# Optimization experiments

Hardware: AMD Instinct MI355X
Metric: run time of the kernel (lower is better)

## Reference

```python
import jax, jax.numpy as jnp
import numpy as np

N_HEAD = 16
HEAD_DIM = 64
N_EMBD = N_HEAD * HEAD_DIM
KS, STRIDE = 4, 4
LN_EPS = 1e-5


def _layernorm(x, g, b):
    mu = jnp.mean(x, axis=-1, keepdims=True)
    var = jnp.var(x, axis=-1, keepdims=True)
    return (x - mu) * jax.lax.rsqrt(var + LN_EPS) * g + b


def _depthwise_conv(x_bcl, w):
    # x_bcl: [N, head_dim, L], w: [head_dim, 1, KS] (torch Conv1d groups=head_dim layout)
    return jax.lax.conv_general_dilated(
        x_bcl, w, window_strides=(STRIDE,), padding='VALID',
        dimension_numbers=('NCH', 'OIH', 'NCH'), feature_group_count=HEAD_DIM)


def setup_inputs() -> dict:
    key = jax.random.key(0)
    ks = jax.random.split(key, 12)
    B, T, L = 8, 64, 4096
    s = 0.02
    return {
        'x': jax.random.normal(ks[0], (B, T, N_EMBD), jnp.float32),
        'cached_k': jax.random.normal(ks[1], (B, N_HEAD, L, HEAD_DIM), jnp.float32),
        'cached_v': jax.random.normal(ks[2], (B, N_HEAD, L, HEAD_DIM), jnp.float32),
        'w_attn': jax.random.normal(ks[3], (N_EMBD, 3 * N_EMBD), jnp.float32) * s,
        'b_attn': jnp.zeros((3 * N_EMBD,), jnp.float32),
        'w_proj': jax.random.normal(ks[4], (N_EMBD, N_EMBD), jnp.float32) * s,
        'b_proj': jnp.zeros((N_EMBD,), jnp.float32),
        'k_conv': jax.random.normal(ks[5], (HEAD_DIM, 1, KS), jnp.float32) * 0.5,
        'v_conv': jax.random.normal(ks[6], (HEAD_DIM, 1, KS), jnp.float32) * 0.5,
        'ln_k_g': jnp.ones((HEAD_DIM,), jnp.float32),
        'ln_k_b': jnp.zeros((HEAD_DIM,), jnp.float32),
        'ln_v_g': jnp.ones((HEAD_DIM,), jnp.float32),
        'ln_v_b': jnp.zeros((HEAD_DIM,), jnp.float32),
    }


def reference(x, cached_k, cached_v, w_attn, b_attn, w_proj, b_proj,
              k_conv, v_conv, ln_k_g, ln_k_b, ln_v_g, ln_v_b):
    B, T, C = x.shape
    H, hd = N_HEAD, HEAD_DIM
    qkv = x @ w_attn + b_attn                      # [B,T,3C]
    q, k, v = jnp.split(qkv, 3, axis=-1)
    q = q.reshape(B, T, H, hd).transpose(0, 2, 1, 3)  # [B,H,T,hd]
    k = k.reshape(B, T, H, hd).transpose(0, 2, 1, 3)
    v = v.reshape(B, T, H, hd).transpose(0, 2, 1, 3)

    # compress cached K/V: depthwise conv over cache length, then LayerNorm
    L = cached_k.shape[2]
    pk = cached_k.transpose(0, 1, 3, 2).reshape(B * H, hd, L)
    pv = cached_v.transpose(0, 1, 3, 2).reshape(B * H, hd, L)
    ck = _depthwise_conv(pk, k_conv).reshape(B, H, hd, -1).transpose(0, 1, 3, 2)  # [B,H,Lc,hd]
    cv = _depthwise_conv(pv, v_conv).reshape(B, H, hd, -1).transpose(0, 1, 3, 2)
    ck = jax.lax.stop_gradient(_layernorm(ck, ln_k_g, ln_k_b))
    cv = jax.lax.stop_gradient(_layernorm(cv, ln_v_g, ln_v_b))

    k_full = jnp.concatenate([ck, k], axis=2)      # [B,H,Tk,hd]
    v_full = jnp.concatenate([cv, v], axis=2)
    Tk = k_full.shape[2]

    # faithful to original: rectangular tril(T, Tk) -> query i sees keys j<=i
    mask = jnp.tril(jnp.ones((T, Tk), dtype=bool))
    att = jnp.einsum('bhqd,bhkd->bhqk', q, k_full) * (1.0 / np.sqrt(hd))
    att = jnp.where(mask[None, None], att, -jnp.inf)
    att = jax.nn.softmax(att, axis=-1)
    y = jnp.einsum('bhqk,bhkd->bhqd', att, v_full)
    y = y.transpose(0, 2, 1, 3).reshape(B, T, C)
    return y @ w_proj + b_proj
```

## Files before the change

### kernel.cpp

```cpp
#include <hip/hip_runtime.h>
#include <math.h>

#define NH 16
#define LCACHE 4096

typedef __attribute__((ext_vector_type(8))) short short8;
typedef __attribute__((ext_vector_type(8))) unsigned short ushort8;
typedef __attribute__((ext_vector_type(4))) float f32x4;

__device__ __forceinline__ unsigned short f2bf(float f) {
    unsigned int u = __float_as_uint(f);
    u = (u + 0x7fffu + ((u >> 16) & 1u)) >> 16;
    return (unsigned short)u;
}

__global__ __launch_bounds__(256)
void prep_kernel(const float* __restrict__ cached_k, const float* __restrict__ cached_v,
                 const float* __restrict__ kcw, const float* __restrict__ vcw,
                 const float* __restrict__ lkg, const float* __restrict__ lkb,
                 const float* __restrict__ lvg, const float* __restrict__ lvb,
                 const float* __restrict__ x, const float* __restrict__ w_attn,
                 const float* __restrict__ w_proj,
                 ushort* __restrict__ ckf, ushort* __restrict__ cvtf,
                 ushort* __restrict__ xp, ushort* __restrict__ wq,
                 ushort* __restrict__ wp)
{
    __shared__ float Wt[64][65];
    const int bid = blockIdx.x, tid = threadIdx.x;
    const int w = tid >> 6, l = tid & 63;

    const int bh = bid >> 2, sub = bid & 3;
    const int T = sub >> 1, half = sub & 1;
    const float* S = (T ? cached_v : cached_k) + (size_t)bh * (LCACHE * 64);
    float tap[8][4];
#pragma unroll
    for (int rq = 0; rq < 8; ++rq) {
        int key = half * 32 + w * 8 + rq;
        const float* p = S + (size_t)key * 256 + l;
        tap[rq][0] = p[0]; tap[rq][1] = p[64]; tap[rq][2] = p[128]; tap[rq][3] = p[192];
    }

    const int isP = (bid >= 256);
    const int g2  = bid & 255;
    const int ntw = g2 >> 4, ktw = g2 & 15;
    const float* W = isP ? w_proj : w_attn;
    const int ldw  = isP ? 1024 : 3072;
    ushort* D      = isP ? wp : wq;
    float wreg[16];
#pragma unroll
    for (int rep = 0; rep < 16; ++rep) {
        int lin = rep * 256 + tid;
        int kr = lin >> 6, nn = lin & 63;
        wreg[rep] = W[(size_t)(ktw * 64 + kr) * ldw + ntw * 64 + nn];
    }

    {
        const float* cwp = T ? vcw : kcw;
        float4 w4v = *(const float4*)(cwp + l * 4);
        float g = (T ? lvg : lkg)[l], bb = (T ? lvb : lkb)[l];
        ushort* dstf = (T ? cvtf : ckf) + (size_t)bh * 4096;
#pragma unroll
        for (int it = 0; it < 2; ++it) {
            float av[4];
#pragma unroll
            for (int q = 0; q < 4; ++q) {
                int rq = it * 4 + q;
                float acc = tap[rq][0] * w4v.x;
                acc = fmaf(tap[rq][1], w4v.y, acc);
                acc = fmaf(tap[rq][2], w4v.z, acc);
                acc = fmaf(tap[rq][3], w4v.w, acc);
                av[q] = acc;
            }
            float s1[4], s2[4];
#pragma unroll
            for (int q = 0; q < 4; ++q) { s1[q] = av[q]; s2[q] = av[q] * av[q]; }
#pragma unroll
            for (int o = 32; o; o >>= 1) {
#pragma unroll
                for (int q = 0; q < 4; ++q) {
                    s1[q] += __shfl_xor(s1[q], o);
                    s2[q] += __shfl_xor(s2[q], o);
                }
            }
#pragma unroll
            for (int q = 0; q < 4; ++q) {
                int key = half * 32 + w * 8 + it * 4 + q;
                float mu  = s1[q] * 0.015625f;
                float var = s2[q] * 0.015625f - mu * mu;
                float outv = (av[q] - mu) * rsqrtf(var + 1e-5f) * g + bb;
                const int d = l;
                int off;
                if (T)
                    off = ((d >> 4) * 2 + (key >> 5)) * 512
                        + ((key >> 3) & 3) * 128 + (d & 15) * 8 + (key & 7);
                else
                    off = ((key >> 4) * 2 + (d >> 5)) * 512
                        + ((d >> 3) & 3) * 128 + (key & 15) * 8 + (d & 7);
                dstf[off] = f2bf(outv);
            }
        }
    }

    {
#pragma unroll
        for (int rep = 0; rep < 16; ++rep) {
            int lin = rep * 256 + tid;
            Wt[lin >> 6][lin & 63] = wreg[rep];
        }
        __syncthreads();
        int r = l & 15, kg8 = l >> 4;
#pragma unroll
        for (int e = 0; e < 2; ++e) {
            int bi = w + e * 4;
            int kb = bi >> 2, nb = bi & 3;
            ushort8 o;
#pragma unroll
            for (int j = 0; j < 8; ++j)
                o[j] = f2bf(Wt[kb * 32 + kg8 * 8 + j][nb * 16 + r]);
            size_t f_lin = (size_t)(ntw * 16 + ktw) * 8 + bi;
            *(ushort8*)(D + f_lin * 512 + l * 8) = o;
        }
    }

    if (bid < 64) {
        int r = l & 15, kg8 = l >> 4;
#pragma unroll
        for (int i = 0; i < 4; ++i) {
            int f = bid * 16 + w * 4 + i;
            int mt = f >> 6, kt = (f >> 2) & 15, fi = f & 3;
            int kb = fi >> 1, mb = fi & 1;
            int m  = mt * 32 + mb * 16 + r;
            int k0 = kt * 64 + kb * 32 + kg8 * 8;
            const float* s = x + (size_t)m * 1024 + k0;
            ushort8 o;
#pragma unroll
            for (int j = 0; j < 8; ++j) o[j] = f2bf(s[j]);
            *(ushort8*)(xp + (size_t)f * 512 + l * 8) = o;
        }
    }
}

__global__ __launch_bounds__(512, 2)
void attn_kernel(const ushort* __restrict__ ckf, const ushort* __restrict__ cvtf,
                 const float* __restrict__ b_attn,
                 const ushort* __restrict__ xp, const ushort* __restrict__ wq,
                 ushort* __restrict__ yp)
{
    __shared__ __align__(16) float qs[32][68];
    __shared__ __align__(16) ushort P_lds[32 * 64];

    const int bid = blockIdx.x;
    const int h    = ((bid & 7) << 1) | ((bid >> 3) & 1);
    const int rem  = bid >> 4;
    const int b    = rem >> 1;
    const int half = rem & 1;
    const int mtA  = b * 2 + half;

    const int tid = threadIdx.x;
    const int w = tid >> 6, l = tid & 63;
    const int kg = w >> 2, w4 = w & 3;
    const int c = l & 15, rg = l >> 4;
    const int g = w & 1, dup = w >> 1;

    const ushort* ckb = ckf + (size_t)(b * NH + h) * 4096;
    const ushort* cvb = cvtf + (size_t)(b * NH + h) * 4096;
    short8 akf[4][2];
#pragma unroll
    for (int mf = 0; mf < 4; ++mf)
#pragma unroll
        for (int kf = 0; kf < 2; ++kf)
            akf[mf][kf] = *(const short8*)(ckb + (mf * 2 + kf) * 512 + l * 8);
    short8 avf[2];
#pragma unroll
    for (int kf = 0; kf < 2; ++kf)
        avf[kf] = *(const short8*)(cvb + (dup * 2 + kf) * 512 + l * 8);

    const ushort* ab = xp + (size_t)mtA * 32768;
    const ushort* bb = wq + (size_t)h * 65536;
    f32x4 acc0 = {0.f,0.f,0.f,0.f}, acc1 = {0.f,0.f,0.f,0.f};
#pragma unroll
    for (int s = 0; s < 8; ++s) {
        const int kt = kg * 8 + s;
        const ushort* A = ab + kt * 2048;
        const ushort* B = bb + kt * 4096;
        short8 a00 = *(const short8*)(A + l * 8);
        short8 a01 = *(const short8*)(A + 512 + l * 8);
        short8 a10 = *(const short8*)(A + 1024 + l * 8);
        short8 a11 = *(const short8*)(A + 1536 + l * 8);
        short8 b0  = *(const short8*)(B + (size_t)w4 * 512 + l * 8);
        short8 b1  = *(const short8*)(B + (size_t)(4 + w4) * 512 + l * 8);
        acc0 = __builtin_amdgcn_mfma_f32_16x16x32_bf16(a00, b0, acc0, 0, 0, 0);
        acc1 = __builtin_amdgcn_mfma_f32_16x16x32_bf16(a01, b0, acc1, 0, 0, 0);
        acc0 = __builtin_amdgcn_mfma_f32_16x16x32_bf16(a10, b1, acc0, 0, 0, 0);
        acc1 = __builtin_amdgcn_mfma_f32_16x16x32_bf16(a11, b1, acc1, 0, 0, 0);
    }

    {
        const int n = w4 * 16 + c;
        if (kg == 0) {
#pragma unroll
            for (int mb = 0; mb < 2; ++mb) {
                f32x4 acc = mb ? acc1 : acc0;
#pragma unroll
                for (int rr = 0; rr < 4; ++rr)
                    qs[mb * 16 + rg * 4 + rr][n] = acc[rr];
            }
        }
        __syncthreads();
        if (kg == 1) {
            float bv = b_attn[h * 64 + n];
#pragma unroll
            for (int mb = 0; mb < 2; ++mb) {
                f32x4 acc = mb ? acc1 : acc0;
#pragma unroll
                for (int rr = 0; rr < 4; ++rr) {
                    int m = mb * 16 + rg * 4 + rr;
                    qs[m][n] = (qs[m][n] + acc[rr] + bv) * 0.125f;
                }
            }
        }
        __syncthreads();
    }

    short8 qb[2];
#pragma unroll
    for (int kf = 0; kf < 2; ++kf) {
        int row = 16 * g + c;
        int d0  = 32 * kf + 8 * rg;
        float4 v0 = *(const float4*)&qs[row][d0];
        float4 v1 = *(const float4*)&qs[row][d0 + 4];
        ushort8 t;
        t[0] = f2bf(v0.x); t[1] = f2bf(v0.y); t[2] = f2bf(v0.z); t[3] = f2bf(v0.w);
        t[4] = f2bf(v1.x); t[5] = f2bf(v1.y); t[6] = f2bf(v1.z); t[7] = f2bf(v1.w);
        qb[kf] = (short8)t;
    }

    f32x4 sacc[4];
#pragma unroll
    for (int mf = 0; mf < 4; ++mf) { sacc[mf][0]=0.f; sacc[mf][1]=0.f; sacc[mf][2]=0.f; sacc[mf][3]=0.f; }
#pragma unroll
    for (int mf = 0; mf < 4; ++mf) {
        sacc[mf] = __builtin_amdgcn_mfma_f32_16x16x32_bf16(akf[mf][0], qb[0], sacc[mf], 0, 0, 0);
        sacc[mf] = __builtin_amdgcn_mfma_f32_16x16x32_bf16(akf[mf][1], qb[1], sacc[mf], 0, 0, 0);
    }

    const int gq = half * 32 + 16 * g + c;
    float pv[4][4];
    float mx = -3.0e38f;
#pragma unroll
    for (int mf = 0; mf < 4; ++mf)
#pragma unroll
        for (int rr = 0; rr < 4; ++rr) {
            int kidx = 16 * mf + 4 * rg + rr;
            float sc = (kidx <= gq) ? sacc[mf][rr] : -3.0e38f;
            pv[mf][rr] = sc;
            mx = fmaxf(mx, sc);
        }
    mx = fmaxf(mx, __shfl_xor(mx, 16));
    mx = fmaxf(mx, __shfl_xor(mx, 32));
    float sum = 0.f;
#pragma unroll
    for (int mf = 0; mf < 4; ++mf)
#pragma unroll
        for (int rr = 0; rr < 4; ++rr) {
            int kidx = 16 * mf + 4 * rg + rr;
            float e = (kidx <= gq) ? __expf(pv[mf][rr] - mx) : 0.f;
            pv[mf][rr] = e;
            sum += e;
        }
    sum += __shfl_xor(sum, 16);
    sum += __shfl_xor(sum, 32);
    float inv = 1.0f / sum;

    if (dup == 0) {
        int q = 16 * g + c;
        int swz = (q & 7) << 3;
#pragma unroll
        for (int mf = 0; mf < 4; ++mf)
#pragma unroll
            for (int rr = 0; rr < 4; ++rr) {
                int kidx = 16 * mf + 4 * rg + rr;
                P_lds[q * 64 + (kidx ^ swz)] = f2bf(pv[mf][rr] * inv);
            }
    }
    __syncthreads();

    short8 pb[2];
#pragma unroll
    for (int kf = 0; kf < 2; ++kf) {
        int q = 16 * g + c;
        int key0 = 32 * kf + 8 * rg;
        pb[kf] = *(const short8*)&P_lds[q * 64 + (key0 ^ ((q & 7) << 3))];
    }
    f32x4 oacc = {0.f, 0.f, 0.f, 0.f};
    oacc = __builtin_amdgcn_mfma_f32_16x16x32_bf16(avf[0], pb[0], oacc, 0, 0, 0);
    oacc = __builtin_amdgcn_mfma_f32_16x16x32_bf16(avf[1], pb[1], oacc, 0, 0, 0);

#pragma unroll
    for (int rr = 0; rr < 4; ++rr) {
        int d  = 16 * dup + 4 * rg + rr;
        int kb = d >> 5, ke = d & 31;
        int l2 = ((ke >> 3) << 4) | c;
        int j2 = ke & 7;
        size_t off = (size_t)mtA * 32768 + (size_t)h * 2048
                   + (size_t)(kb * 2 + g) * 512 + (size_t)l2 * 8 + j2;
        yp[off] = f2bf(oacc[rr]);
    }
}

__global__ __launch_bounds__(512, 2)
void gemm2_kernel(const ushort* __restrict__ Ap, const ushort* __restrict__ Bp,
                  const float* __restrict__ bias, float* __restrict__ C)
{
    __shared__ float red[32][68];

    const int bid = blockIdx.x;
    const int nt = ((bid & 7) << 1) | ((bid >> 3) & 1);
    const int mt = bid >> 4;
    const int tid = threadIdx.x;
    const int w = tid >> 6, l = tid & 63;
    const int kg = w >> 2, w4 = w & 3;
    const int c = l & 15, rg = l >> 4;

    const ushort* ab = Ap + (size_t)mt * 32768;
    const ushort* bb = Bp + (size_t)nt * 65536;
    f32x4 acc0 = {0.f,0.f,0.f,0.f}, acc1 = {0.f,0.f,0.f,0.f};
#pragma unroll
    for (int s = 0; s < 8; ++s) {
        const int kt = kg * 8 + s;
        const ushort* A = ab + kt * 2048;
        const ushort* B = bb + kt * 4096;
        short8 a00 = *(const short8*)(A + l * 8);
        short8 a01 = *(const short8*)(A + 512 + l * 8);
        short8 a10 = *(const short8*)(A + 1024 + l * 8);
        short8 a11 = *(const short8*)(A + 1536 + l * 8);
        short8 b0  = *(const short8*)(B + (size_t)w4 * 512 + l * 8);
        short8 b1  = *(const short8*)(B + (size_t)(4 + w4) * 512 + l * 8);
        acc0 = __builtin_amdgcn_mfma_f32_16x16x32_bf16(a00, b0, acc0, 0, 0, 0);
        acc1 = __builtin_amdgcn_mfma_f32_16x16x32_bf16(a01, b0, acc1, 0, 0, 0);
        acc0 = __builtin_amdgcn_mfma_f32_16x16x32_bf16(a10, b1, acc0, 0, 0, 0);
        acc1 = __builtin_amdgcn_mfma_f32_16x16x32_bf16(a11, b1, acc1, 0, 0, 0);
    }

    const int nl = w4 * 16 + c;
    if (kg == 0) {
#pragma unroll
        for (int mb = 0; mb < 2; ++mb) {
            f32x4 acc = mb ? acc1 : acc0;
#pragma unroll
            for (int rr = 0; rr < 4; ++rr)
                red[mb * 16 + rg * 4 + rr][nl] = acc[rr];
        }
    }
    __syncthreads();
    if (kg == 1) {
        float bv = bias[nt * 64 + nl];
#pragma unroll
        for (int mb = 0; mb < 2; ++mb) {
            f32x4 acc = mb ? acc1 : acc0;
#pragma unroll
            for (int rr = 0; rr < 4; ++rr) {
                int m = mb * 16 + rg * 4 + rr;
                C[(size_t)(mt * 32 + m) * 1024 + nt * 64 + nl] =
                    red[m][nl] + acc[rr] + bv;
            }
        }
    }
}

extern "C" void kernel_launch(void* const* d_in, const int* in_sizes, int n_in,
                              void* d_out, int out_size, void* d_ws, size_t ws_size,
                              hipStream_t stream)
{
    const float* x        = (const float*)d_in[0];
    const float* cached_k = (const float*)d_in[1];
    const float* cached_v = (const float*)d_in[2];
    const float* w_attn   = (const float*)d_in[3];
    const float* b_attn   = (const float*)d_in[4];
    const float* w_proj   = (const float*)d_in[5];
    const float* b_proj   = (const float*)d_in[6];
    const float* k_conv   = (const float*)d_in[7];
    const float* v_conv   = (const float*)d_in[8];
    const float* ln_k_g   = (const float*)d_in[9];
    const float* ln_k_b   = (const float*)d_in[10];
    const float* ln_v_g   = (const float*)d_in[11];
    const float* ln_v_b   = (const float*)d_in[12];

    ushort* xp   = (ushort*)d_ws;
    ushort* wq   = xp + 524288;
    ushort* wp   = wq + 1048576;
    ushort* yp   = wp + 1048576;
    ushort* ckf  = yp + 524288;
    ushort* cvtf = ckf + 524288;
    float* out   = (float*)d_out;

    prep_kernel<<<512, 256, 0, stream>>>(cached_k, cached_v, k_conv, v_conv,
                                         ln_k_g, ln_k_b, ln_v_g, ln_v_b,
                                         x, w_attn, w_proj, ckf, cvtf, xp, wq, wp);
    attn_kernel<<<256, 512, 0, stream>>>(ckf, cvtf, b_attn, xp, wq, yp);
    gemm2_kernel<<<256, 512, 0, stream>>>(yp, wp, b_proj, out);
}
```

Baseline: 26.88 us.

## Fuse cache conv+LayerNorm into attention kernel, overlapped with Q projection

Moves the depthwise conv and LayerNorm of the cached K/V into the attention kernel. Half the warps compute the compressed keys directly into LDS while the other half compute the Q projection GEMM over the full K dimension, so the split-K reduction through shared memory goes away. Each block computes only the rows it needs (32 or 64 keys depending on half), which removes the global round-trip of the packed ckf/cvtf buffers. The prep kernel becomes a pure weight and activation packing kernel with separate blocks for x. In exchange it adds 16 KB of LDS per block and gives each GEMM warp twice the serial K loop.

```diff
diff --git a/kernel.cpp b/kernel.cpp
--- a/kernel.cpp
+++ b/kernel.cpp
@@ -15,13 +15,8 @@
 }
 
 __global__ __launch_bounds__(256)
-void prep_kernel(const float* __restrict__ cached_k, const float* __restrict__ cached_v,
-                 const float* __restrict__ kcw, const float* __restrict__ vcw,
-                 const float* __restrict__ lkg, const float* __restrict__ lkb,
-                 const float* __restrict__ lvg, const float* __restrict__ lvb,
-                 const float* __restrict__ x, const float* __restrict__ w_attn,
+void pack_kernel(const float* __restrict__ x, const float* __restrict__ w_attn,
                  const float* __restrict__ w_proj,
-                 ushort* __restrict__ ckf, ushort* __restrict__ cvtf,
                  ushort* __restrict__ xp, ushort* __restrict__ wq,
                  ushort* __restrict__ wp)
 {
@@ -29,83 +24,18 @@
     const int bid = blockIdx.x, tid = threadIdx.x;
     const int w = tid >> 6, l = tid & 63;
 
-    const int bh = bid >> 2, sub = bid & 3;
-    const int T = sub >> 1, half = sub & 1;
-    const float* S = (T ? cached_v : cached_k) + (size_t)bh * (LCACHE * 64);
-    float tap[8][4];
-#pragma unroll
-    for (int rq = 0; rq < 8; ++rq) {
-        int key = half * 32 + w * 8 + rq;
-        const float* p = S + (size_t)key * 256 + l;
-        tap[rq][0] = p[0]; tap[rq][1] = p[64]; tap[rq][2] = p[128]; tap[rq][3] = p[192];
-    }
-
-    const int isP = (bid >= 256);
-    const int g2  = bid & 255;
-    const int ntw = g2 >> 4, ktw = g2 & 15;
-    const float* W = isP ? w_proj : w_attn;
-    const int ldw  = isP ? 1024 : 3072;
-    ushort* D      = isP ? wp : wq;
-    float wreg[16];
-#pragma unroll
-    for (int rep = 0; rep < 16; ++rep) {
-        int lin = rep * 256 + tid;
-        int kr = lin >> 6, nn = lin & 63;
-        wreg[rep] = W[(size_t)(ktw * 64 + kr) * ldw + ntw * 64 + nn];
-    }
-
-    {
-        const float* cwp = T ? vcw : kcw;
-        float4 w4v = *(const float4*)(cwp + l * 4);
-        float g = (T ? lvg : lkg)[l], bb = (T ? lvb : lkb)[l];
-        ushort* dstf = (T ? cvtf : ckf) + (size_t)bh * 4096;
-#pragma unroll
-        for (int it = 0; it < 2; ++it) {
-            float av[4];
-#pragma unroll
-            for (int q = 0; q < 4; ++q) {
-                int rq = it * 4 + q;
-                float acc = tap[rq][0] * w4v.x;
-                acc = fmaf(tap[rq][1], w4v.y, acc);
-                acc = fmaf(tap[rq][2], w4v.z, acc);
-                acc = fmaf(tap[rq][3], w4v.w, acc);
-                av[q] = acc;
-            }
-            float s1[4], s2[4];
-#pragma unroll
-            for (int q = 0; q < 4; ++q) { s1[q] = av[q]; s2[q] = av[q] * av[q]; }
-#pragma unroll
-            for (int o = 32; o; o >>= 1) {
-#pragma unroll
-                for (int q = 0; q < 4; ++q) {
-                    s1[q] += __shfl_xor(s1[q], o);
-                    s2[q] += __shfl_xor(s2[q], o);
-                }
-            }
-#pragma unroll
-            for (int q = 0; q < 4; ++q) {
-                int key = half * 32 + w * 8 + it * 4 + q;
-                float mu  = s1[q] * 0.015625f;
-                float var = s2[q] * 0.015625f - mu * mu;
-                float outv = (av[q] - mu) * rsqrtf(var + 1e-5f) * g + bb;
-                const int d = l;
-                int off;
-                if (T)
-                    off = ((d >> 4) * 2 + (key >> 5)) * 512
-                        + ((key >> 3) & 3) * 128 + (d & 15) * 8 + (key & 7);
-                else
-                    off = ((key >> 4) * 2 + (d >> 5)) * 512
-                        + ((d >> 3) & 3) * 128 + (key & 15) * 8 + (d & 7);
-                dstf[off] = f2bf(outv);
-            }
-        }
-    }
-
-    {
+    if (bid < 512) {
+        const int isP = (bid >= 256);
+        const int g2  = bid & 255;
+        const int ntw = g2 >> 4, ktw = g2 & 15;
+        const float* W = isP ? w_proj : w_attn;
+        const int ldw  = isP ? 1024 : 3072;
+        ushort* D      = isP ? wp : wq;
 #pragma unroll
         for (int rep = 0; rep < 16; ++rep) {
             int lin = rep * 256 + tid;
-            Wt[lin >> 6][lin & 63] = wreg[rep];
+            int kr = lin >> 6, nn = lin & 63;
+            Wt[kr][nn] = W[(size_t)(ktw * 64 + kr) * ldw + ntw * 64 + nn];
         }
         __syncthreads();
         int r = l & 15, kg8 = l >> 4;
@@ -120,13 +50,15 @@
             size_t f_lin = (size_t)(ntw * 16 + ktw) * 8 + bi;
             *(ushort8*)(D + f_lin * 512 + l * 8) = o;
         }
-    }
-
-    if (bid < 64) {
+        return;
+    }
+
+    {
+        int bid2 = bid - 512;
         int r = l & 15, kg8 = l >> 4;
 #pragma unroll
         for (int i = 0; i < 4; ++i) {
-            int f = bid * 16 + w * 4 + i;
+            int f = bid2 * 16 + w * 4 + i;
             int mt = f >> 6, kt = (f >> 2) & 15, fi = f & 3;
             int kb = fi >> 1, mb = fi & 1;
             int m  = mt * 32 + mb * 16 + r;
@@ -141,13 +73,18 @@
 }
 
 __global__ __launch_bounds__(512, 2)
-void attn_kernel(const ushort* __restrict__ ckf, const ushort* __restrict__ cvtf,
+void attn_kernel(const float* __restrict__ cached_k, const float* __restrict__ cached_v,
+                 const float* __restrict__ kcw, const float* __restrict__ vcw,
+                 const float* __restrict__ lkg, const float* __restrict__ lkb,
+                 const float* __restrict__ lvg, const float* __restrict__ lvb,
                  const float* __restrict__ b_attn,
                  const ushort* __restrict__ xp, const ushort* __restrict__ wq,
                  ushort* __restrict__ yp)
 {
     __shared__ __align__(16) float qs[32][68];
-    __shared__ __align__(16) ushort P_lds[32 * 64];
+    __shared__ __align__(16) ushort P_lds[2048];
+    __shared__ __align__(16) ushort ckf_s[4096];
+    __shared__ __align__(16) ushort cvf_s[4096];
 
     const int bid = blockIdx.x;
     const int h    = ((bid & 7) << 1) | ((bid >> 3) & 1);
@@ -158,69 +95,115 @@
 
     const int tid = threadIdx.x;
     const int w = tid >> 6, l = tid & 63;
-    const int kg = w >> 2, w4 = w & 3;
     const int c = l & 15, rg = l >> 4;
     const int g = w & 1, dup = w >> 1;
 
-    const ushort* ckb = ckf + (size_t)(b * NH + h) * 4096;
-    const ushort* cvb = cvtf + (size_t)(b * NH + h) * 4096;
+    {
+        ushort8 z = {0,0,0,0,0,0,0,0};
+        ((ushort8*)ckf_s)[tid] = z;
+        ((ushort8*)cvf_s)[tid] = z;
+    }
+    __syncthreads();
+
+    if (w >= 4) {
+        const int cw = w - 4;
+        const int NR = half ? 64 : 32;
+        const float* Kb = cached_k + (size_t)(b * NH + h) * (LCACHE * 64);
+        const float* Vb = cached_v + (size_t)(b * NH + h) * (LCACHE * 64);
+        float4 wk = *(const float4*)(kcw + l * 4);
+        float4 wv = *(const float4*)(vcw + l * 4);
+        float gk = lkg[l], bk = lkb[l], gv = lvg[l], bv = lvb[l];
+
+        const int iters = (2 * NR) / 4;
+        for (int it = 0; it < iters; it += 4) {
+            float tap[4][4]; int isKv[4], lcv[4];
+#pragma unroll
+            for (int q = 0; q < 4; ++q) {
+                int t = cw + (it + q) * 4;
+                isKv[q] = (t < NR);
+                int lc = isKv[q] ? t : t - NR;
+                lcv[q] = lc;
+                const float* p = (isKv[q] ? Kb : Vb) + (size_t)lc * 256 + l;
+                tap[q][0] = p[0]; tap[q][1] = p[64]; tap[q][2] = p[128]; tap[q][3] = p[192];
+            }
+            float av[4], s1[4], s2[4];
+#pragma unroll
+            for (int q = 0; q < 4; ++q) {
+                float4 cwv = isKv[q] ? wk : wv;
+                float a = tap[q][0] * cwv.x;
+                a = fmaf(tap[q][1], cwv.y, a);
+                a = fmaf(tap[q][2], cwv.z, a);
+                a = fmaf(tap[q][3], cwv.w, a);
+                av[q] = a; s1[q] = a; s2[q] = a * a;
+            }
+#pragma unroll
+            for (int o = 32; o; o >>= 1) {
+#pragma unroll
+                for (int q = 0; q < 4; ++q) {
+                    s1[q] += __shfl_xor(s1[q], o);
+                    s2[q] += __shfl_xor(s2[q], o);
+                }
+            }
+#pragma unroll
+            for (int q = 0; q < 4; ++q) {
+                float mu  = s1[q] * 0.015625f;
+                float var = s2[q] * 0.015625f - mu * mu;
+                float gg = isKv[q] ? gk : gv, bb2 = isKv[q] ? bk : bv;
+                float outv = (av[q] - mu) * rsqrtf(var + 1e-5f) * gg + bb2;
+                unsigned short bf = f2bf(outv);
+                int key = lcv[q], d = l;
+                if (isKv[q]) {
+                    int off = ((key >> 4) * 2 + (d >> 5)) * 512
+                            + ((d >> 3) & 3) * 128 + (key & 15) * 8 + (d & 7);
+                    ckf_s[off] = bf;
+                } else {
+                    int off = ((d >> 4) * 2 + (key >> 5)) * 512
+                            + ((key >> 3) & 3) * 128 + (d & 15) * 8 + (key & 7);
+                    cvf_s[off] = bf;
+                }
+            }
+        }
+    } else {
+        const ushort* ab = xp + (size_t)mtA * 32768;
+        const ushort* bb = wq + (size_t)h * 65536;
+        f32x4 acc0 = {0.f,0.f,0.f,0.f}, acc1 = {0.f,0.f,0.f,0.f};
+#pragma unroll
+        for (int kt = 0; kt < 16; ++kt) {
+            const ushort* A = ab + kt * 2048;
+            const ushort* B = bb + kt * 4096;
+            short8 a00 = *(const short8*)(A + l * 8);
+            short8 a01 = *(const short8*)(A + 512 + l * 8);
+            short8 a10 = *(const short8*)(A + 1024 + l * 8);
+            short8 a11 = *(const short8*)(A + 1536 + l * 8);
+            short8 b0  = *(const short8*)(B + (size_t)w * 512 + l * 8);
+            short8 b1  = *(const short8*)(B + (size_t)(4 + w) * 512 + l * 8);
+            acc0 = __builtin_amdgcn_mfma_f32_16x16x32_bf16(a00, b0, acc0, 0, 0, 0);
+            acc1 = __builtin_amdgcn_mfma_f32_16x16x32_bf16(a01, b0, acc1, 0, 0, 0);
+            acc0 = __builtin_amdgcn_mfma_f32_16x16x32_bf16(a10, b1, acc0, 0, 0, 0);
+            acc1 = __builtin_amdgcn_mfma_f32_16x16x32_bf16(a11, b1, acc1, 0, 0, 0);
+        }
+        const int n = w * 16 + c;
+        float bv2 = b_attn[h * 64 + n];
+#pragma unroll
+        for (int mb = 0; mb < 2; ++mb) {
+            f32x4 acc = mb ? acc1 : acc0;
+#pragma unroll
+            for (int rr = 0; rr < 4; ++rr)
+                qs[mb * 16 + rg * 4 + rr][n] = (acc[rr] + bv2) * 0.125f;
+        }
+    }
+    __syncthreads();
+
     short8 akf[4][2];
 #pragma unroll
     for (int mf = 0; mf < 4; ++mf)
 #pragma unroll
         for (int kf = 0; kf < 2; ++kf)
-            akf[mf][kf] = *(const short8*)(ckb + (mf * 2 + kf) * 512 + l * 8);
+            akf[mf][kf] = *(const short8*)&ckf_s[(mf * 2 + kf) * 512 + l * 8];
     short8 avf[2];
 #pragma unroll
     for (int kf = 0; kf < 2; ++kf)
-        avf[kf] = *(const short8*)(cvb + (dup * 2 + kf) * 512 + l * 8);
-
-    const ushort* ab = xp + (size_t)mtA * 32768;
-    const ushort* bb = wq + (size_t)h * 65536;
-    f32x4 acc0 = {0.f,0.f,0.f,0.f}, acc1 = {0.f,0.f,0.f,0.f};
-#pragma unroll
-    for (int s = 0; s < 8; ++s) {
-        const int kt = kg * 8 + s;
-        const ushort* A = ab + kt * 2048;
-        const ushort* B = bb + kt * 4096;
-        short8 a00 = *(const short8*)(A + l * 8);
-        short8 a01 = *(const short8*)(A + 512 + l * 8);
-        short8 a10 = *(const short8*)(A + 1024 + l * 8);
-        short8 a11 = *(const short8*)(A + 1536 + l * 8);
-        short8 b0  = *(const short8*)(B + (size_t)w4 * 512 + l * 8);
-        short8 b1  = *(const short8*)(B + (size_t)(4 + w4) * 512 + l * 8);
-        acc0 = __builtin_amdgcn_mfma_f32_16x16x32_bf16(a00, b0, acc0, 0, 0, 0);
-        acc1 = __builtin_amdgcn_mfma_f32_16x16x32_bf16(a01, b0, acc1, 0, 0, 0);
-        acc0 = __builtin_amdgcn_mfma_f32_16x16x32_bf16(a10, b1, acc0, 0, 0, 0);
-        acc1 = __builtin_amdgcn_mfma_f32_16x16x32_bf16(a11, b1, acc1, 0, 0, 0);
-    }
-
-    {
-        const int n = w4 * 16 + c;
-        if (kg == 0) {
-#pragma unroll
-            for (int mb = 0; mb < 2; ++mb) {
-                f32x4 acc = mb ? acc1 : acc0;
-#pragma unroll
-                for (int rr = 0; rr < 4; ++rr)
-                    qs[mb * 16 + rg * 4 + rr][n] = acc[rr];
-            }
-        }
-        __syncthreads();
-        if (kg == 1) {
-            float bv = b_attn[h * 64 + n];
-#pragma unroll
-            for (int mb = 0; mb < 2; ++mb) {
-                f32x4 acc = mb ? acc1 : acc0;
-#pragma unroll
-                for (int rr = 0; rr < 4; ++rr) {
-                    int m = mb * 16 + rg * 4 + rr;
-                    qs[m][n] = (qs[m][n] + acc[rr] + bv) * 0.125f;
-                }
-            }
-        }
-        __syncthreads();
-    }
+        avf[kf] = *(const short8*)&cvf_s[(dup * 2 + kf) * 512 + l * 8];
 
     short8 qb[2];
 #pragma unroll
@@ -386,17 +369,15 @@
     const float* ln_v_g   = (const float*)d_in[11];
     const float* ln_v_b   = (const float*)d_in[12];
 
-    ushort* xp   = (ushort*)d_ws;
-    ushort* wq   = xp + 524288;
-    ushort* wp   = wq + 1048576;
-    ushort* yp   = wp + 1048576;
-    ushort* ckf  = yp + 524288;
-    ushort* cvtf = ckf + 524288;
-    float* out   = (float*)d_out;
-
-    prep_kernel<<<512, 256, 0, stream>>>(cached_k, cached_v, k_conv, v_conv,
+    ushort* xp = (ushort*)d_ws;
+    ushort* wq = xp + 524288;
+    ushort* wp = wq + 1048576;
+    ushort* yp = wp + 1048576;
+    float* out = (float*)d_out;
+
+    pack_kernel<<<576, 256, 0, stream>>>(x, w_attn, w_proj, xp, wq, wp);
+    attn_kernel<<<256, 512, 0, stream>>>(cached_k, cached_v, k_conv, v_conv,
                                          ln_k_g, ln_k_b, ln_v_g, ln_v_b,
-                                         x, w_attn, w_proj, ckf, cvtf, xp, wq, wp);
-    attn_kernel<<<256, 512, 0, stream>>>(ckf, cvtf, b_attn, xp, wq, yp);
+                                         b_attn, xp, wq, yp);
     gemm2_kernel<<<256, 512, 0, stream>>>(yp, wp, b_proj, out);
 }
```

Measured after the change: 30.09 us. 1.12x slower.

## Split prep and output-projection work across twice as many blocks

Applied to the files above, without the earlier changes.

The prep kernel now launches 1024 blocks, each handling a quarter of the keys, half of a weight tile, and one x fragment per block, so the x conversion is spread across blocks instead of piled onto the first 64. The output-projection GEMM launches 512 blocks with 32-column tiles and a four-way K split, reduced through shared memory. The bf16 conversion switches to the HIP intrinsic. The goal is more parallelism and better latency hiding on a small problem, at the cost of more blocks and a wider reduction.

```diff
diff --git a/kernel.cpp b/kernel.cpp
--- a/kernel.cpp
+++ b/kernel.cpp
@@ -1,4 +1,5 @@
 #include <hip/hip_runtime.h>
+#include <hip/hip_bf16.h>
 #include <math.h>
 
 #define NH 16
@@ -9,12 +10,13 @@
 typedef __attribute__((ext_vector_type(4))) float f32x4;
 
 __device__ __forceinline__ unsigned short f2bf(float f) {
-    unsigned int u = __float_as_uint(f);
-    u = (u + 0x7fffu + ((u >> 16) & 1u)) >> 16;
-    return (unsigned short)u;
+    __hip_bfloat16 b = __float2bfloat16(f);
+    unsigned short u;
+    __builtin_memcpy(&u, &b, 2);
+    return u;
 }
 
-__global__ __launch_bounds__(256)
+__global__ __launch_bounds__(256, 4)
 void prep_kernel(const float* __restrict__ cached_k, const float* __restrict__ cached_v,
                  const float* __restrict__ kcw, const float* __restrict__ vcw,
                  const float* __restrict__ lkg, const float* __restrict__ lkb,
@@ -25,33 +27,47 @@
                  ushort* __restrict__ xp, ushort* __restrict__ wq,
                  ushort* __restrict__ wp)
 {
-    __shared__ float Wt[64][65];
+    __shared__ float Wt[32][65];
     const int bid = blockIdx.x, tid = threadIdx.x;
     const int w = tid >> 6, l = tid & 63;
 
-    const int bh = bid >> 2, sub = bid & 3;
-    const int T = sub >> 1, half = sub & 1;
+    const int bh = bid >> 3, sub = bid & 7;
+    const int T = sub >> 2, quarter = sub & 3;
     const float* S = (T ? cached_v : cached_k) + (size_t)bh * (LCACHE * 64);
-    float tap[8][4];
-#pragma unroll
-    for (int rq = 0; rq < 8; ++rq) {
-        int key = half * 32 + w * 8 + rq;
+    float tap[4][4];
+#pragma unroll
+    for (int q = 0; q < 4; ++q) {
+        int key = quarter * 16 + w * 4 + q;
         const float* p = S + (size_t)key * 256 + l;
-        tap[rq][0] = p[0]; tap[rq][1] = p[64]; tap[rq][2] = p[128]; tap[rq][3] = p[192];
-    }
-
-    const int isP = (bid >= 256);
-    const int g2  = bid & 255;
-    const int ntw = g2 >> 4, ktw = g2 & 15;
+        tap[q][0] = p[0]; tap[q][1] = p[64]; tap[q][2] = p[128]; tap[q][3] = p[192];
+    }
+
+    const int isP = bid >> 9;
+    const int rem = bid & 511;
+    const int ntw = rem >> 5, ktw = (rem >> 1) & 15, kbh = rem & 1;
     const float* W = isP ? w_proj : w_attn;
     const int ldw  = isP ? 1024 : 3072;
     ushort* D      = isP ? wp : wq;
-    float wreg[16];
-#pragma unroll
-    for (int rep = 0; rep < 16; ++rep) {
+    float wreg[8];
+#pragma unroll
+    for (int rep = 0; rep < 8; ++rep) {
         int lin = rep * 256 + tid;
         int kr = lin >> 6, nn = lin & 63;
-        wreg[rep] = W[(size_t)(ktw * 64 + kr) * ldw + ntw * 64 + nn];
+        wreg[rep] = W[(size_t)(ktw * 64 + kbh * 32 + kr) * ldw + ntw * 64 + nn];
+    }
+
+    const int doX = (w == (bid & 3));
+    float xr[8];
+    if (doX) {
+        int f = bid;
+        int mt = f >> 6, kt = (f >> 2) & 15, fi = f & 3;
+        int kb = fi >> 1, mb = fi & 1;
+        int r = l & 15, kg8 = l >> 4;
+        int m  = mt * 32 + mb * 16 + r;
+        int k0 = kt * 64 + kb * 32 + kg8 * 8;
+        const float* s = x + (size_t)m * 1024 + k0;
+#pragma unroll
+        for (int j = 0; j < 8; ++j) xr[j] = s[j];
     }
 
     {
@@ -59,84 +75,63 @@
         float4 w4v = *(const float4*)(cwp + l * 4);
         float g = (T ? lvg : lkg)[l], bb = (T ? lvb : lkb)[l];
         ushort* dstf = (T ? cvtf : ckf) + (size_t)bh * 4096;
-#pragma unroll
-        for (int it = 0; it < 2; ++it) {
-            float av[4];
+        float av[4], s1[4], s2[4];
+#pragma unroll
+        for (int q = 0; q < 4; ++q) {
+            float a = tap[q][0] * w4v.x;
+            a = fmaf(tap[q][1], w4v.y, a);
+            a = fmaf(tap[q][2], w4v.z, a);
+            a = fmaf(tap[q][3], w4v.w, a);
+            av[q] = a; s1[q] = a; s2[q] = a * a;
+        }
+#pragma unroll
+        for (int o = 32; o; o >>= 1) {
 #pragma unroll
             for (int q = 0; q < 4; ++q) {
-                int rq = it * 4 + q;
-                float acc = tap[rq][0] * w4v.x;
-                acc = fmaf(tap[rq][1], w4v.y, acc);
-                acc = fmaf(tap[rq][2], w4v.z, acc);
-                acc = fmaf(tap[rq][3], w4v.w, acc);
-                av[q] = acc;
+                s1[q] += __shfl_xor(s1[q], o);
+                s2[q] += __shfl_xor(s2[q], o);
             }
-            float s1[4], s2[4];
-#pragma unroll
-            for (int q = 0; q < 4; ++q) { s1[q] = av[q]; s2[q] = av[q] * av[q]; }
-#pragma unroll
-            for (int o = 32; o; o >>= 1) {
-#pragma unroll
-                for (int q = 0; q < 4; ++q) {
-                    s1[q] += __shfl_xor(s1[q], o);
-                    s2[q] += __shfl_xor(s2[q], o);
-                }
-            }
-#pragma unroll
-            for (int q = 0; q < 4; ++q) {
-                int key = half * 32 + w * 8 + it * 4 + q;
-                float mu  = s1[q] * 0.015625f;
-                float var = s2[q] * 0.015625f - mu * mu;
-                float outv = (av[q] - mu) * rsqrtf(var + 1e-5f) * g + bb;
-                const int d = l;
-                int off;
-                if (T)
-                    off = ((d >> 4) * 2 + (key >> 5)) * 512
-                        + ((key >> 3) & 3) * 128 + (d & 15) * 8 + (key & 7);
-                else
-                    off = ((key >> 4) * 2 + (d >> 5)) * 512
-                        + ((d >> 3) & 3) * 128 + (key & 15) * 8 + (d & 7);
-                dstf[off] = f2bf(outv);
-            }
+        }
+#pragma unroll
+        for (int q = 0; q < 4; ++q) {
+            int key = quarter * 16 + w * 4 + q;
+            float mu  = s1[q] * 0.015625f;
+            float var = s2[q] * 0.015625f - mu * mu;
+            float outv = (av[q] - mu) * rsqrtf(var + 1e-5f) * g + bb;
+            unsigned short bf = f2bf(outv);
+            const int d = l;
+            int off;
+            if (T)
+                off = ((d >> 4) * 2 + (key >> 5)) * 512
+                    + ((key >> 3) & 3) * 128 + (d & 15) * 8 + (key & 7);
+            else
+                off = ((key >> 4) * 2 + (d >> 5)) * 512
+                    + ((d >> 3) & 3) * 128 + (key & 15) * 8 + (d & 7);
+            dstf[off] = bf;
         }
     }
 
     {
 #pragma unroll
-        for (int rep = 0; rep < 16; ++rep) {
+        for (int rep = 0; rep < 8; ++rep) {
             int lin = rep * 256 + tid;
             Wt[lin >> 6][lin & 63] = wreg[rep];
         }
         __syncthreads();
         int r = l & 15, kg8 = l >> 4;
-#pragma unroll
-        for (int e = 0; e < 2; ++e) {
-            int bi = w + e * 4;
-            int kb = bi >> 2, nb = bi & 3;
-            ushort8 o;
-#pragma unroll
-            for (int j = 0; j < 8; ++j)
-                o[j] = f2bf(Wt[kb * 32 + kg8 * 8 + j][nb * 16 + r]);
-            size_t f_lin = (size_t)(ntw * 16 + ktw) * 8 + bi;
-            *(ushort8*)(D + f_lin * 512 + l * 8) = o;
-        }
-    }
-
-    if (bid < 64) {
-        int r = l & 15, kg8 = l >> 4;
-#pragma unroll
-        for (int i = 0; i < 4; ++i) {
-            int f = bid * 16 + w * 4 + i;
-            int mt = f >> 6, kt = (f >> 2) & 15, fi = f & 3;
-            int kb = fi >> 1, mb = fi & 1;
-            int m  = mt * 32 + mb * 16 + r;
-            int k0 = kt * 64 + kb * 32 + kg8 * 8;
-            const float* s = x + (size_t)m * 1024 + k0;
-            ushort8 o;
-#pragma unroll
-            for (int j = 0; j < 8; ++j) o[j] = f2bf(s[j]);
-            *(ushort8*)(xp + (size_t)f * 512 + l * 8) = o;
-        }
+        ushort8 o;
+#pragma unroll
+        for (int j = 0; j < 8; ++j)
+            o[j] = f2bf(Wt[kg8 * 8 + j][w * 16 + r]);
+        size_t f_lin = (size_t)(ntw * 16 + ktw) * 8 + kbh * 4 + w;
+        *(ushort8*)(D + f_lin * 512 + l * 8) = o;
+    }
+
+    if (doX) {
+        ushort8 o;
+#pragma unroll
+        for (int j = 0; j < 8; ++j) o[j] = f2bf(xr[j]);
+        *(ushort8*)(xp + (size_t)bid * 512 + l * 8) = o;
     }
 }
 
@@ -147,7 +142,7 @@
                  ushort* __restrict__ yp)
 {
     __shared__ __align__(16) float qs[32][68];
-    __shared__ __align__(16) ushort P_lds[32 * 64];
+    __shared__ __align__(16) ushort P_lds[2048];
 
     const int bid = blockIdx.x;
     const int h    = ((bid & 7) << 1) | ((bid >> 3) & 1);
@@ -312,57 +307,61 @@
 void gemm2_kernel(const ushort* __restrict__ Ap, const ushort* __restrict__ Bp,
                   const float* __restrict__ bias, float* __restrict__ C)
 {
-    __shared__ float red[32][68];
+    __shared__ float red[3][2][32][18];
 
     const int bid = blockIdx.x;
-    const int nt = ((bid & 7) << 1) | ((bid >> 3) & 1);
-    const int mt = bid >> 4;
+    const int xcd = bid & 7, idx = bid >> 3;
+    const int nt2 = xcd * 4 + (idx & 3);
+    const int mt  = idx >> 2;
+    const int nt  = nt2 >> 1;
     const int tid = threadIdx.x;
     const int w = tid >> 6, l = tid & 63;
-    const int kg = w >> 2, w4 = w & 3;
+    const int kg = w >> 1, nb2 = w & 1;
+    const int nb = (nt2 & 1) * 2 + nb2;
     const int c = l & 15, rg = l >> 4;
 
     const ushort* ab = Ap + (size_t)mt * 32768;
     const ushort* bb = Bp + (size_t)nt * 65536;
     f32x4 acc0 = {0.f,0.f,0.f,0.f}, acc1 = {0.f,0.f,0.f,0.f};
 #pragma unroll
-    for (int s = 0; s < 8; ++s) {
-        const int kt = kg * 8 + s;
+    for (int s = 0; s < 4; ++s) {
+        const int kt = kg * 4 + s;
         const ushort* A = ab + kt * 2048;
         const ushort* B = bb + kt * 4096;
         short8 a00 = *(const short8*)(A + l * 8);
         short8 a01 = *(const short8*)(A + 512 + l * 8);
         short8 a10 = *(const short8*)(A + 1024 + l * 8);
         short8 a11 = *(const short8*)(A + 1536 + l * 8);
-        short8 b0  = *(const short8*)(B + (size_t)w4 * 512 + l * 8);
-        short8 b1  = *(const short8*)(B + (size_t)(4 + w4) * 512 + l * 8);
+        short8 b0  = *(const short8*)(B + (size_t)nb * 512 + l * 8);
+        short8 b1  = *(const short8*)(B + (size_t)(4 + nb) * 512 + l * 8);
         acc0 = __builtin_amdgcn_mfma_f32_16x16x32_bf16(a00, b0, acc0, 0, 0, 0);
         acc1 = __builtin_amdgcn_mfma_f32_16x16x32_bf16(a01, b0, acc1, 0, 0, 0);
         acc0 = __builtin_amdgcn_mfma_f32_16x16x32_bf16(a10, b1, acc0, 0, 0, 0);
         acc1 = __builtin_amdgcn_mfma_f32_16x16x32_bf16(a11, b1, acc1, 0, 0, 0);
     }
 
-    const int nl = w4 * 16 + c;
-    if (kg == 0) {
+    if (kg > 0) {
 #pragma unroll
         for (int mb = 0; mb < 2; ++mb) {
             f32x4 acc = mb ? acc1 : acc0;
 #pragma unroll
             for (int rr = 0; rr < 4; ++rr)
-                red[mb * 16 + rg * 4 + rr][nl] = acc[rr];
+                red[kg - 1][nb2][mb * 16 + rg * 4 + rr][c] = acc[rr];
         }
     }
     __syncthreads();
-    if (kg == 1) {
-        float bv = bias[nt * 64 + nl];
+    if (kg == 0) {
+        const int n = nt2 * 32 + nb2 * 16 + c;
+        float bv = bias[n];
 #pragma unroll
         for (int mb = 0; mb < 2; ++mb) {
             f32x4 acc = mb ? acc1 : acc0;
 #pragma unroll
             for (int rr = 0; rr < 4; ++rr) {
                 int m = mb * 16 + rg * 4 + rr;
-                C[(size_t)(mt * 32 + m) * 1024 + nt * 64 + nl] =
-                    red[m][nl] + acc[rr] + bv;
+                float v = acc[rr] + red[0][nb2][m][c] + red[1][nb2][m][c]
+                        + red[2][nb2][m][c] + bv;
+                C[(size_t)(mt * 32 + m) * 1024 + n] = v;
             }
         }
     }
@@ -394,9 +393,9 @@
     ushort* cvtf = ckf + 524288;
     float* out   = (float*)d_out;
 
-    prep_kernel<<<512, 256, 0, stream>>>(cached_k, cached_v, k_conv, v_conv,
-                                         ln_k_g, ln_k_b, ln_v_g, ln_v_b,
-                                         x, w_attn, w_proj, ckf, cvtf, xp, wq, wp);
+    prep_kernel<<<1024, 256, 0, stream>>>(cached_k, cached_v, k_conv, v_conv,
+                                          ln_k_g, ln_k_b, ln_v_g, ln_v_b,
+                                          x, w_attn, w_proj, ckf, cvtf, xp, wq, wp);
     attn_kernel<<<256, 512, 0, stream>>>(ckf, cvtf, b_attn, xp, wq, yp);
-    gemm2_kernel<<<256, 512, 0, stream>>>(yp, wp, b_proj, out);
+    gemm2_kernel<<<512, 512, 0, stream>>>(yp, wp, b_proj, out);
 }
```

Result: faster. 25.83 us (-3.9%).
